# Kernel tuning notes

Hardware: AMD Instinct MI355X
Metric: run time of the kernel (lower is better)

## Reference

```python
import jax, jax.numpy as jnp
import numpy as np

GX, GY, GZ = 128, 128, 16   # voxel_range
N = 100000                  # occupied voxels
C = 64                      # channels (inc == outc)
K = 27                      # 3x3x3 kernel offsets
EPS = 1e-5
NEG_SLOPE = 0.01            # LeakyReLU default


def _kernel_map():
    """Build sparse-conv neighbor map: nbr[k, n] = row index of the input voxel at
    coord[n] + offset[k], or N (sentinel -> zero feature) if unoccupied/out of range."""
    rng = np.random.RandomState(0)
    flat = rng.choice(GX * GY * GZ, size=N, replace=False)
    x = flat // (GY * GZ)
    rem = flat % (GY * GZ)
    y = rem // GZ
    z = rem % GZ
    lut = np.full(GX * GY * GZ, N, dtype=np.int32)
    lut[flat] = np.arange(N, dtype=np.int32)
    offs = [(i, j, k) for i in (-1, 0, 1) for j in (-1, 0, 1) for k in (-1, 0, 1)]
    nbr = np.full((K, N), N, dtype=np.int32)
    for ki, (dx, dy, dz) in enumerate(offs):
        xs, ys, zs = x + dx, y + dy, z + dz
        valid = (xs >= 0) & (xs < GX) & (ys >= 0) & (ys < GY) & (zs >= 0) & (zs < GZ)
        fl = (np.clip(xs, 0, GX - 1) * (GY * GZ)
              + np.clip(ys, 0, GY - 1) * GZ
              + np.clip(zs, 0, GZ - 1))
        nbr[ki] = np.where(valid, lut[fl], N)
    return jnp.asarray(nbr)


def setup_inputs() -> dict:
    key = jax.random.key(0)
    k0, k1, k2 = jax.random.split(key, 3)
    w_scale = 1.0 / np.sqrt(C * K)  # Minkowski-style fan-in init
    return {
        "feats": jax.random.normal(k0, (N, C), jnp.float32),
        "W1": jax.random.normal(k1, (K, C, C), jnp.float32) * w_scale,
        "g1": jnp.ones((C,), jnp.float32),
        "b1": jnp.zeros((C,), jnp.float32),
        "W2": jax.random.normal(k2, (K, C, C), jnp.float32) * w_scale,
        "g2": jnp.ones((C,), jnp.float32),
        "b2": jnp.zeros((C,), jnp.float32),
        "nbr_idx": _kernel_map(),
    }


def _sparse_conv(f, W, nbr):
    # gather-GEMM-scatter: fp has a zero sentinel row at index N
    fp = jnp.concatenate([f, jnp.zeros((1, f.shape[1]), f.dtype)], axis=0)
    g = fp[nbr]                                # [K, N, Cin] gathered neighbors
    return jnp.einsum('knc,kco->no', g, W)     # [N, Cout]


def _bn(x, gamma, beta):
    # training-mode BatchNorm over all active voxels, per channel
    m = jnp.mean(x, axis=0)
    v = jnp.var(x, axis=0)
    return (x - m) * jax.lax.rsqrt(v + EPS) * gamma + beta


def _lrelu(x):
    return jnp.where(x >= 0, x, NEG_SLOPE * x)


def reference(feats, W1, g1, b1, W2, g2, b2, nbr_idx):
    skip = feats  # downsample is identity (inc == outc, stride == 1)
    y = _lrelu(_bn(_sparse_conv(feats, W1, nbr_idx), g1, b1))
    y = _lrelu(_bn(_sparse_conv(y, W2, nbr_idx), g2, b2))
    return _lrelu(skip + y)
```

## Files before the change

### kernel.cpp

```cpp
#include <hip/hip_runtime.h>
#include <hip/hip_bf16.h>


#define N_VOX 100000
#define NCH 64
#define NK 27
#define ROWS 128
#define NBLK ((N_VOX + ROWS - 1) / ROWS)

typedef __hip_bfloat16 bf16;
typedef __attribute__((ext_vector_type(8))) short bf16x8;
typedef __attribute__((ext_vector_type(4))) float f32x4;

__device__ __forceinline__ float b2f(short s) {
  unsigned u = ((unsigned)(unsigned short)s) << 16;
  return __builtin_bit_cast(float, u);
}
__device__ __forceinline__ short f2b(float f) {
  __hip_bfloat16 h = __float2bfloat16(f);
  return __builtin_bit_cast(short, h);
}

__device__ __forceinline__ void gload16(const void* g, void* l) {
  __builtin_amdgcn_global_load_lds(
      (const __attribute__((address_space(1))) void*)g,
      (__attribute__((address_space(3))) void*)l, 16, 0, 0);
}

__global__ void cast_feats(const float* __restrict__ feats, bf16* __restrict__ fbf) {
  const size_t i = ((size_t)blockIdx.x * 256 + threadIdx.x) * 8;
  if (i >= (size_t)(N_VOX + 1) * NCH) return;
  bf16x8 o;
  if (i < (size_t)N_VOX * NCH) {
    const f32x4 v0 = *reinterpret_cast<const f32x4*>(feats + i);
    const f32x4 v1 = *reinterpret_cast<const f32x4*>(feats + i + 4);
#pragma unroll
    for (int e = 0; e < 8; ++e) o[e] = f2b(e < 4 ? v0[e] : v1[e - 4]);
  } else {
#pragma unroll
    for (int e = 0; e < 8; ++e) o[e] = 0;
  }
  *reinterpret_cast<bf16x8*>((short*)fbf + i) = o;
}

__global__ void pack_w(const float* __restrict__ W1, const float* __restrict__ W2,
                       bf16* __restrict__ wp1, bf16* __restrict__ wp2) {
  const int t = blockIdx.x * 256 + threadIdx.x;
  const int half = NK * 4 * 2 * 64;
  if (t >= 2 * half) return;
  const float* W = (t < half) ? W1 : W2;
  short* wp = (short*)((t < half) ? wp1 : wp2);
  const int q = (t < half) ? t : t - half;
  const int l  = q & 63;
  const int kb = (q >> 6) & 1;
  const int j  = (q >> 7) & 3;
  const int k  = q >> 9;
  const int oo = j * 16 + (l & 15);
  const int c0 = kb * 32 + (l >> 4) * 8;
  bf16x8 v;
#pragma unroll
  for (int e = 0; e < 8; ++e)
    v[e] = f2b(W[((size_t)k * 64 + c0 + e) * 64 + oo]);
  *reinterpret_cast<bf16x8*>(&wp[(size_t)q * 8]) = v;
}

__global__ __launch_bounds__(256, 3)
void conv_mfma(const bf16* __restrict__ feat, const bf16* __restrict__ wp,
               const int* __restrict__ nbr, bf16* __restrict__ y,
               float* __restrict__ part) {
  __shared__ short GB[3][4096];
  __shared__ int nbrL[NK * ROWS];
  __shared__ float redS[4][NCH];
  __shared__ float redQ[4][NCH];

  const int tid = threadIdx.x;
  const int lane = tid & 63;
  const int wv = tid >> 6;

  const int nwg = NBLK;
  const int xcd = blockIdx.x & 7;
  const int pos = blockIdx.x >> 3;
  const int q8 = nwg >> 3, r8 = nwg & 7;
  const int bid = (xcd < r8 ? xcd * (q8 + 1) : r8 * (q8 + 1) + (xcd - r8) * q8) + pos;
  const int n0 = bid * ROWS;

  for (int t = tid; t < NK * ROWS; t += 256) {
    const int k = t >> 7;
    const int rr = t & (ROWS - 1);
    nbrL[t] = (n0 + rr < N_VOX) ? nbr[(size_t)k * N_VOX + n0 + rr] : N_VOX;
  }
  __syncthreads();

  const int r0 = wv * 32 + (lane & 15);
  const int koff = (lane >> 4) * 8;

  f32x4 acc[2][4];
#pragma unroll
  for (int h = 0; h < 2; ++h)
#pragma unroll
    for (int j = 0; j < 4; ++j)
      acc[h][j] = (f32x4){0.f, 0.f, 0.f, 0.f};

  bf16x8 AE[4], AO[4];

#define LOAD_A(A, k)                                                        \
  {                                                                         \
    const int i0 = nbrL[(k) * ROWS + r0];                                   \
    const int i1 = nbrL[(k) * ROWS + r0 + 16];                              \
    A[0] = *reinterpret_cast<const bf16x8*>(feat + (size_t)i0 * 64 + koff); \
    A[1] = *reinterpret_cast<const bf16x8*>(feat + (size_t)i0 * 64 + 32 + koff); \
    A[2] = *reinterpret_cast<const bf16x8*>(feat + (size_t)i1 * 64 + koff); \
    A[3] = *reinterpret_cast<const bf16x8*>(feat + (size_t)i1 * 64 + 32 + koff); \
  }

#define STAGE_B(slot, k)                                                    \
  {                                                                         \
    const short* srcb = (const short*)wp + (size_t)(k) * 4096 +             \
                        (wv * 2) * 512 + lane * 8;                          \
    gload16((const void*)srcb, (void*)&GB[slot][(wv * 2) * 512]);           \
    gload16((const void*)(srcb + 512), (void*)&GB[slot][(wv * 2 + 1) * 512]); \
  }

#define MFMA_TAP(A, B)                                                      \
  _Pragma("unroll")                                                         \
  for (int h = 0; h < 2; ++h)                                               \
    _Pragma("unroll")                                                       \
    for (int j = 0; j < 4; ++j)                                             \
      _Pragma("unroll")                                                     \
      for (int kb = 0; kb < 2; ++kb)                                        \
        acc[h][j] = __builtin_amdgcn_mfma_f32_16x16x32_bf16(                \
            A[h * 2 + kb], B[j * 2 + kb], acc[h][j], 0, 0, 0);

#define TILE_STEP(Acur, Aoth, t)                                            \
  {                                                                         \
    if ((t) < NK - 1) { asm volatile("s_waitcnt vmcnt(2)" ::: "memory"); }  \
    else              { asm volatile("s_waitcnt vmcnt(0)" ::: "memory"); }  \
    __builtin_amdgcn_sched_barrier(0);                                      \
    __builtin_amdgcn_s_barrier();                                           \
    if ((t) + 1 < NK) LOAD_A(Aoth, (t) + 1)                                 \
    if ((t) + 2 < NK) {                                                     \
      const int stslot = ((t) + 2) % 3;                                     \
      STAGE_B(stslot, (t) + 2)                                              \
    }                                                                       \
    __builtin_amdgcn_sched_barrier(0);       \
    bf16x8 Bf[8];                                                           \
    const int rdslot = (t) % 3;                                             \
    _Pragma("unroll")                                                       \
    for (int f = 0; f < 8; ++f)                                             \
      Bf[f] = *reinterpret_cast<const bf16x8*>(                             \
          &GB[rdslot][f * 512 + lane * 8]);                                 \
    MFMA_TAP(Acur, Bf)                                                      \
  }

  STAGE_B(0, 0)
  LOAD_A(AE, 0)
  STAGE_B(1, 1)

#pragma unroll 1
  for (int j = 0; j < 13; ++j) {
    const int t = 2 * j;
    TILE_STEP(AE, AO, t)
    TILE_STEP(AO, AE, t + 1)
  }
  TILE_STEP(AE, AO, 26)

#undef LOAD_A
#undef STAGE_B
#undef MFMA_TAP
#undef TILE_STEP

  __syncthreads();
  {
    short* Ys = &GB[0][0];
#pragma unroll
    for (int h = 0; h < 2; ++h)
#pragma unroll
      for (int j = 0; j < 4; ++j) {
        const int col = j * 16 + (lane & 15);
#pragma unroll
        for (int r = 0; r < 4; ++r) {
          const int lrow = wv * 32 + h * 16 + (lane >> 4) * 4 + r;
          Ys[lrow * 64 + col] = f2b(acc[h][j][r]);
        }
      }
    __syncthreads();
#pragma unroll
    for (int pth = 0; pth < 4; ++pth) {
      const int c = pth * 256 + tid;
      const int grow = n0 + (c >> 3);
      if (grow < N_VOX) {
        const bf16x8 v = *reinterpret_cast<const bf16x8*>(&Ys[c * 8]);
        *reinterpret_cast<bf16x8*>((short*)y + (size_t)grow * 64 + (c & 7) * 8) = v;
      }
    }
  }

#pragma unroll
  for (int j = 0; j < 4; ++j) {
    float s1 = 0.f, s2 = 0.f;
#pragma unroll
    for (int h = 0; h < 2; ++h)
#pragma unroll
      for (int r = 0; r < 4; ++r) {
        const float v = acc[h][j][r];
        s1 += v;
        s2 += v * v;
      }
    s1 += __shfl_xor(s1, 16); s2 += __shfl_xor(s2, 16);
    s1 += __shfl_xor(s1, 32); s2 += __shfl_xor(s2, 32);
    if (lane < 16) {
      redS[wv][j * 16 + lane] = s1;
      redQ[wv][j * 16 + lane] = s2;
    }
  }
  __syncthreads();
  if (tid < NCH) {
    const float s1 = redS[0][tid] + redS[1][tid] + redS[2][tid] + redS[3][tid];
    const float s2 = redQ[0][tid] + redQ[1][tid] + redQ[2][tid] + redQ[3][tid];
    part[(size_t)blockIdx.x * 128 + tid] = s1;
    part[(size_t)blockIdx.x * 128 + 64 + tid] = s2;
  }
}

__global__ void finalize(const float* __restrict__ part, int nblk,
                         const float* __restrict__ g, const float* __restrict__ b,
                         float* __restrict__ ab) {
  __shared__ float r1[256], r2[256];
  const int c = blockIdx.x;
  const int t = threadIdx.x;
  float s1 = 0.f, s2 = 0.f;
  for (int bb = t; bb < nblk; bb += 256) {
    s1 += part[(size_t)bb * 128 + c];
    s2 += part[(size_t)bb * 128 + 64 + c];
  }
  r1[t] = s1; r2[t] = s2;
  __syncthreads();
  for (int off = 128; off > 0; off >>= 1) {
    if (t < off) { r1[t] += r1[t + off]; r2[t] += r2[t + off]; }
    __syncthreads();
  }
  if (t == 0) {
    const float m = r1[0] / (float)N_VOX;
    const float v = r2[0] / (float)N_VOX - m * m;
    const float a = g[c] * rsqrtf(v + 1e-5f);
    const float sh = b[c] - m * a;
    ab[c] = a;
    ab[64 + c] = sh;
  }
}

__global__ void bn_act(const bf16* __restrict__ y, const float* __restrict__ ab,
                       bf16* __restrict__ z) {
  const size_t i = ((size_t)blockIdx.x * 256 + threadIdx.x) * 8;
  if (i >= (size_t)(N_VOX + 1) * NCH) return;
  const int col = (int)(i & 63);
  bf16x8 o;
  if (i < (size_t)N_VOX * NCH) {
    const bf16x8 v = *reinterpret_cast<const bf16x8*>((const short*)y + i);
#pragma unroll
    for (int e = 0; e < 8; ++e) {
      float x = b2f(v[e]) * ab[col + e] + ab[64 + col + e];
      x = x < 0.f ? 0.01f * x : x;
      o[e] = f2b(x);
    }
  } else {
#pragma unroll
    for (int e = 0; e < 8; ++e) o[e] = 0;
  }
  *reinterpret_cast<bf16x8*>((short*)z + i) = o;
}

__global__ void bn_act_res(const bf16* __restrict__ y, const float* __restrict__ ab,
                           const float* __restrict__ feats, float* __restrict__ out) {
  const size_t i = ((size_t)blockIdx.x * 256 + threadIdx.x) * 8;
  const int col = (int)(i & 63);
  const bf16x8 v = *reinterpret_cast<const bf16x8*>((const short*)y + i);
  const f32x4 s0 = *reinterpret_cast<const f32x4*>(feats + i);
  const f32x4 s1 = *reinterpret_cast<const f32x4*>(feats + i + 4);
  f32x4 o0, o1;
#pragma unroll
  for (int e = 0; e < 8; ++e) {
    float x = b2f(v[e]) * ab[col + e] + ab[64 + col + e];
    x = x < 0.f ? 0.01f * x : x;
    float r = (e < 4 ? s0[e] : s1[e - 4]) + x;
    r = r < 0.f ? 0.01f * r : r;
    if (e < 4) o0[e] = r; else o1[e - 4] = r;
  }
  *reinterpret_cast<f32x4*>(out + i) = o0;
  *reinterpret_cast<f32x4*>(out + i + 4) = o1;
}

extern "C" void kernel_launch(void* const* d_in, const int* in_sizes, int n_in,
                              void* d_out, int out_size, void* d_ws, size_t ws_size,
                              hipStream_t stream) {
  const float* feats = (const float*)d_in[0];
  const float* W1 = (const float*)d_in[1];
  const float* g1 = (const float*)d_in[2];
  const float* b1 = (const float*)d_in[3];
  const float* W2 = (const float*)d_in[4];
  const float* g2 = (const float*)d_in[5];
  const float* b2 = (const float*)d_in[6];
  const int* nbr = (const int*)d_in[7];
  float* out = (float*)d_out;

  char* p = (char*)d_ws;
  bf16* fbf = (bf16*)p; p += (size_t)(N_VOX + 1) * NCH * 2;
  bf16* ybf = (bf16*)p; p += (size_t)N_VOX * NCH * 2;
  bf16* z = (bf16*)p;   p += (size_t)(N_VOX + 1) * NCH * 2;
  bf16* wp1 = (bf16*)p; p += 442368;
  bf16* wp2 = (bf16*)p; p += 442368;
  float* part = (float*)p; p += (size_t)NBLK * 128 * 4;
  float* ab1 = (float*)p; p += 512;
  float* ab2 = (float*)p; p += 512;

  const int cast_blocks = (int)(((size_t)(N_VOX + 1) * NCH / 8 + 255) / 256);

  cast_feats<<<cast_blocks, 256, 0, stream>>>(feats, fbf);
  pack_w<<<108, 256, 0, stream>>>(W1, W2, wp1, wp2);

  conv_mfma<<<NBLK, 256, 0, stream>>>(fbf, wp1, nbr, ybf, part);
  finalize<<<64, 256, 0, stream>>>(part, NBLK, g1, b1, ab1);
  bn_act<<<cast_blocks, 256, 0, stream>>>(ybf, ab1, z);

  conv_mfma<<<NBLK, 256, 0, stream>>>(z, wp2, nbr, ybf, part);
  finalize<<<64, 256, 0, stream>>>(part, NBLK, g2, b2, ab2);
  bn_act_res<<<(N_VOX * NCH / 8) / 256, 256, 0, stream>>>(ybf, ab2, feats, out);
}
```

Measured before the change: 132.8 us.

## Double rows per block to 256 and store conv output directly from registers

```diff
diff --git a/kernel.cpp b/kernel.cpp
--- a/kernel.cpp
+++ b/kernel.cpp
@@ -5,7 +5,7 @@
 #define N_VOX 100000
 #define NCH 64
 #define NK 27
-#define ROWS 128
+#define ROWS 256
 #define NBLK ((N_VOX + ROWS - 1) / ROWS)
 
 typedef __hip_bfloat16 bf16;
@@ -64,7 +64,7 @@
   *reinterpret_cast<bf16x8*>(&wp[(size_t)q * 8]) = v;
 }
 
-__global__ __launch_bounds__(256, 3)
+__global__ __launch_bounds__(256, 2)
 void conv_mfma(const bf16* __restrict__ feat, const bf16* __restrict__ wp,
                const int* __restrict__ nbr, bf16* __restrict__ y,
                float* __restrict__ part) {
@@ -85,32 +85,34 @@
   const int n0 = bid * ROWS;
 
   for (int t = tid; t < NK * ROWS; t += 256) {
-    const int k = t >> 7;
+    const int k = t >> 8;
     const int rr = t & (ROWS - 1);
     nbrL[t] = (n0 + rr < N_VOX) ? nbr[(size_t)k * N_VOX + n0 + rr] : N_VOX;
   }
   __syncthreads();
 
-  const int r0 = wv * 32 + (lane & 15);
+  const int r0 = wv * 64 + (lane & 15);
   const int koff = (lane >> 4) * 8;
 
-  f32x4 acc[2][4];
-#pragma unroll
-  for (int h = 0; h < 2; ++h)
+  f32x4 acc[4][4];
+#pragma unroll
+  for (int g = 0; g < 4; ++g)
 #pragma unroll
     for (int j = 0; j < 4; ++j)
-      acc[h][j] = (f32x4){0.f, 0.f, 0.f, 0.f};
-
-  bf16x8 AE[4], AO[4];
+      acc[g][j] = (f32x4){0.f, 0.f, 0.f, 0.f};
+
+  bf16x8 AE[8], AO[8];
 
 #define LOAD_A(A, k)                                                        \
   {                                                                         \
-    const int i0 = nbrL[(k) * ROWS + r0];                                   \
-    const int i1 = nbrL[(k) * ROWS + r0 + 16];                              \
-    A[0] = *reinterpret_cast<const bf16x8*>(feat + (size_t)i0 * 64 + koff); \
-    A[1] = *reinterpret_cast<const bf16x8*>(feat + (size_t)i0 * 64 + 32 + koff); \
-    A[2] = *reinterpret_cast<const bf16x8*>(feat + (size_t)i1 * 64 + koff); \
-    A[3] = *reinterpret_cast<const bf16x8*>(feat + (size_t)i1 * 64 + 32 + koff); \
+    _Pragma("unroll")                                                       \
+    for (int g = 0; g < 4; ++g) {                                           \
+      const int ig = nbrL[(k) * ROWS + r0 + 16 * g];                        \
+      A[g * 2 + 0] = *reinterpret_cast<const bf16x8*>(                      \
+          feat + (size_t)ig * 64 + koff);                                   \
+      A[g * 2 + 1] = *reinterpret_cast<const bf16x8*>(                      \
+          feat + (size_t)ig * 64 + 32 + koff);                              \
+    }                                                                       \
   }
 
 #define STAGE_B(slot, k)                                                    \
@@ -123,13 +125,13 @@
 
 #define MFMA_TAP(A, B)                                                      \
   _Pragma("unroll")                                                         \
-  for (int h = 0; h < 2; ++h)                                               \
+  for (int g = 0; g < 4; ++g)                                               \
     _Pragma("unroll")                                                       \
     for (int j = 0; j < 4; ++j)                                             \
       _Pragma("unroll")                                                     \
       for (int kb = 0; kb < 2; ++kb)                                        \
-        acc[h][j] = __builtin_amdgcn_mfma_f32_16x16x32_bf16(                \
-            A[h * 2 + kb], B[j * 2 + kb], acc[h][j], 0, 0, 0);
+        acc[g][j] = __builtin_amdgcn_mfma_f32_16x16x32_bf16(                \
+            A[g * 2 + kb], B[j * 2 + kb], acc[g][j], 0, 0, 0);
 
 #define TILE_STEP(Acur, Aoth, t)                                            \
   {                                                                         \
@@ -169,40 +171,26 @@
 #undef MFMA_TAP
 #undef TILE_STEP
 
-  __syncthreads();
-  {
-    short* Ys = &GB[0][0];
-#pragma unroll
-    for (int h = 0; h < 2; ++h)
-#pragma unroll
-      for (int j = 0; j < 4; ++j) {
-        const int col = j * 16 + (lane & 15);
-#pragma unroll
-        for (int r = 0; r < 4; ++r) {
-          const int lrow = wv * 32 + h * 16 + (lane >> 4) * 4 + r;
-          Ys[lrow * 64 + col] = f2b(acc[h][j][r]);
-        }
-      }
-    __syncthreads();
-#pragma unroll
-    for (int pth = 0; pth < 4; ++pth) {
-      const int c = pth * 256 + tid;
-      const int grow = n0 + (c >> 3);
-      if (grow < N_VOX) {
-        const bf16x8 v = *reinterpret_cast<const bf16x8*>(&Ys[c * 8]);
-        *reinterpret_cast<bf16x8*>((short*)y + (size_t)grow * 64 + (c & 7) * 8) = v;
+#pragma unroll
+  for (int g = 0; g < 4; ++g)
+#pragma unroll
+    for (int j = 0; j < 4; ++j) {
+      const int col = j * 16 + (lane & 15);
+#pragma unroll
+      for (int r = 0; r < 4; ++r) {
+        const int row = n0 + wv * 64 + g * 16 + (lane >> 4) * 4 + r;
+        if (row < N_VOX) ((short*)y)[(size_t)row * NCH + col] = f2b(acc[g][j][r]);
       }
     }
-  }
 
 #pragma unroll
   for (int j = 0; j < 4; ++j) {
     float s1 = 0.f, s2 = 0.f;
 #pragma unroll
-    for (int h = 0; h < 2; ++h)
+    for (int g = 0; g < 4; ++g)
 #pragma unroll
       for (int r = 0; r < 4; ++r) {
-        const float v = acc[h][j][r];
+        const float v = acc[g][j][r];
         s1 += v;
         s2 += v * v;
       }
```

New measurement: 129.4 us. 1.03x faster.
